# Performance work log

Measured on AMD Instinct MI355X. Metric: run time of the kernel, lower is better.

## Reference

```python
import jax, jax.numpy as jnp
import numpy as np

B, S, D, H = 4, 2048, 512, 8
DH = D // H  # 64


def setup_inputs() -> dict:
    key = jax.random.key(0)
    ks = jax.random.split(key, 7)
    scale = 1.0 / np.sqrt(D)
    return {
        "in_query": jax.random.normal(ks[0], (B, S, D), dtype=jnp.float32),
        "in_key": jax.random.normal(ks[1], (B, S, D), dtype=jnp.float32),
        "in_value": jax.random.normal(ks[2], (B, S, D), dtype=jnp.float32),
        "W_q": jax.random.normal(ks[3], (D, D), dtype=jnp.float32) * scale,
        "W_k": jax.random.normal(ks[4], (D, D), dtype=jnp.float32) * scale,
        "W_v": jax.random.normal(ks[5], (D, D), dtype=jnp.float32) * scale,
        "W_out": jax.random.normal(ks[6], (D, D), dtype=jnp.float32) * scale,
    }


def _split_heads(x):
    # [B, S, D] -> [B, H, S, DH]
    return x.reshape(B, S, H, DH).transpose(0, 2, 1, 3)


def reference(in_query, in_key, in_value, W_q, W_k, W_v, W_out):
    q = _split_heads(in_query @ W_q)   # [B,H,S,DH]
    k = _split_heads(in_key @ W_k)
    v = _split_heads(in_value @ W_v)
    scores = jnp.einsum("bhqd,bhkd->bhqk", q, k) / jnp.sqrt(jnp.float32(DH))
    attn = jax.nn.softmax(scores, axis=-1)  # dropout p=0 -> identity
    out = jnp.einsum("bhqk,bhkd->bhqd", attn, v)  # [B,H,S,DH]
    out = out.transpose(0, 2, 1, 3).reshape(B, S, D)
    return out @ W_out
```

## Files before the change

### kernel.cpp

```cpp
#include <hip/hip_runtime.h>
#include <hip/hip_bf16.h>
#include <cstdint>
#include <cstddef>


typedef __bf16 bf16;
typedef __attribute__((ext_vector_type(8))) __bf16 bf16x8;
typedef __attribute__((ext_vector_type(4))) __bf16 bf16x4;
typedef __attribute__((ext_vector_type(4))) float floatx4;

#define MFMA16(a, b, c) __builtin_amdgcn_mfma_f32_16x16x32_bf16(a, b, c, 0, 0, 0)

#define GLD16(gp, lp)                                              \
  __builtin_amdgcn_global_load_lds(                                \
      (const __attribute__((address_space(1))) unsigned int*)(gp), \
      (__attribute__((address_space(3))) unsigned int*)(lp), 16, 0, 0)

#define PIPE_TOP()                                     \
  do {                                                 \
    asm volatile("s_waitcnt vmcnt(0)" ::: "memory");   \
    __builtin_amdgcn_s_barrier();                      \
    __builtin_amdgcn_sched_barrier(0);                 \
  } while (0)

#define LGKM_BARRIER()                                 \
  do {                                                 \
    asm volatile("s_waitcnt lgkmcnt(0)" ::: "memory"); \
    __builtin_amdgcn_sched_barrier(0);                 \
    __builtin_amdgcn_s_barrier();                      \
    __builtin_amdgcn_sched_barrier(0);                 \
  } while (0)

__device__ __forceinline__ void split2(float x, bf16& hi, bf16& lo) {
  hi = (bf16)x;
  lo = (bf16)(x - (float)hi);
}

__global__ __launch_bounds__(256) void k_split_w(
    const float* __restrict__ Wq, const float* __restrict__ Wk,
    const float* __restrict__ Wv, const float* __restrict__ Wo,
    bf16* __restrict__ wt_hi, bf16* __restrict__ wt_lo) {
  __shared__ float tile[64][65];
  const int w = blockIdx.z;
  const float* W = (w == 0) ? Wq : (w == 1) ? Wk : (w == 2) ? Wv : Wo;
  const int kb = blockIdx.y * 64, nb = blockIdx.x * 64;
  const int tid = threadIdx.x;
  const int col = tid & 63, rbase = tid >> 6;
#pragma unroll
  for (int i = 0; i < 16; i++) {
    int row = rbase + i * 4;
    tile[row][col] = W[(size_t)(kb + row) * 512 + nb + col];
  }
  __syncthreads();
#pragma unroll
  for (int i = 0; i < 16; i++) {
    int nrow = rbase + i * 4;
    float v = tile[col][nrow];
    bf16 hi, lo;
    split2(v, hi, lo);
    size_t o = (size_t)w * 262144 + (size_t)(nb + nrow) * 512 + (kb + col);
    wt_hi[o] = hi;
    wt_lo[o] = lo;
  }
}

__global__ __launch_bounds__(256) void k_split_x(
    const float* __restrict__ Xq, const float* __restrict__ Xk,
    const float* __restrict__ Xv,
    bf16* __restrict__ Xh, bf16* __restrict__ Xl) {
  const int total = 3 * 1048576;
  for (int j = blockIdx.x * blockDim.x + threadIdx.x; j < total;
       j += gridDim.x * blockDim.x) {
    int w = j >> 20, off = j & 1048575;
    const float* X = (w == 0) ? Xq : (w == 1) ? Xk : Xv;
    floatx4 v = *(const floatx4*)(X + (size_t)off * 4);
    bf16x4 hv, lv;
#pragma unroll
    for (int r = 0; r < 4; r++) {
      bf16 h, l;
      split2(v[r], h, l);
      hv[r] = h; lv[r] = l;
    }
    *(bf16x4*)(Xh + (size_t)w * 4194304 + (size_t)off * 4) = hv;
    *(bf16x4*)(Xl + (size_t)w * 4194304 + (size_t)off * 4) = lv;
  }
}

__global__ __launch_bounds__(256, 3) void k_proj_qkv(
    const bf16* __restrict__ Xh, const bf16* __restrict__ Xl,
    const bf16* __restrict__ wt_hi, const bf16* __restrict__ wt_lo,
    bf16* __restrict__ Q_hi, bf16* __restrict__ Q_lo,
    bf16* __restrict__ K, bf16* __restrict__ Vt) {
  const int P = blockIdx.x;
  const int c_all = P >> 5, within = P & 31;
  const int n_idx = within >> 3, i8 = within & 7;
  const int which = c_all >> 3;
  const int g = ((c_all & 7) << 3) | i8;
  const int m0 = g * 128, n0 = n_idx * 128;

  const uint8_t* Ahb = (const uint8_t*)(Xh + (size_t)which * 4194304);
  const uint8_t* Alb = (const uint8_t*)(Xl + (size_t)which * 4194304);
  const uint8_t* Bhb = (const uint8_t*)(wt_hi + (size_t)which * 262144);
  const uint8_t* Blb = (const uint8_t*)(wt_lo + (size_t)which * 262144);
  const int tid = threadIdx.x, wave = tid >> 6, lane = tid & 63;
  const int l15 = lane & 15, l4 = lane >> 4;
  const int Am0 = (wave & 1) * 64, Bn0 = (wave >> 1) * 64;

  __shared__ bf16 sAh[128 * 32], sAl[128 * 32];
  __shared__ bf16 sBh[128 * 32], sBl[128 * 32];

  int aoff[2], boff[2], dstp[2];
#pragma unroll
  for (int p = 0; p < 2; p++) {
    int slot = p * 256 + tid;
    int row = slot >> 2, phys = slot & 3, lg = phys ^ (row & 3);
    aoff[p] = (m0 + row) * 1024 + lg * 16;
    boff[p] = (n0 + row) * 1024 + lg * 16;
    dstp[p] = slot * 16;
  }

  floatx4 acc[4][4];
#pragma unroll
  for (int i = 0; i < 4; i++)
#pragma unroll
    for (int j = 0; j < 4; j++) acc[i][j] = {0.f, 0.f, 0.f, 0.f};

#pragma unroll
  for (int p = 0; p < 2; p++) {
    GLD16(Ahb + aoff[p], (char*)sAh + dstp[p]);
    GLD16(Alb + aoff[p], (char*)sAl + dstp[p]);
    GLD16(Bhb + boff[p], (char*)sBh + dstp[p]);
    GLD16(Blb + boff[p], (char*)sBl + dstp[p]);
  }

  for (int kb = 0; kb < 512; kb += 32) {
    PIPE_TOP();

    bf16x8 ah[4], al[4], bhf[4], blf[4];
#pragma unroll
    for (int mt = 0; mt < 4; mt++) {
      int row = Am0 + mt * 16 + l15, r3 = row & 3;
      ah[mt] = *(const bf16x8*)((const char*)sAh + row * 64 + ((l4 ^ r3) * 16));
      al[mt] = *(const bf16x8*)((const char*)sAl + row * 64 + ((l4 ^ r3) * 16));
    }
#pragma unroll
    for (int nt = 0; nt < 4; nt++) {
      int row = Bn0 + nt * 16 + l15, r3 = row & 3;
      bhf[nt] = *(const bf16x8*)((const char*)sBh + row * 64 + ((l4 ^ r3) * 16));
      blf[nt] = *(const bf16x8*)((const char*)sBl + row * 64 + ((l4 ^ r3) * 16));
    }

    LGKM_BARRIER();

    if (kb + 32 < 512) {
      const int nkb = kb + 32;
#pragma unroll
      for (int p = 0; p < 2; p++) {
        GLD16(Ahb + aoff[p] + nkb * 2, (char*)sAh + dstp[p]);
        GLD16(Alb + aoff[p] + nkb * 2, (char*)sAl + dstp[p]);
        GLD16(Bhb + boff[p] + nkb * 2, (char*)sBh + dstp[p]);
        GLD16(Blb + boff[p] + nkb * 2, (char*)sBl + dstp[p]);
      }
    }

    __builtin_amdgcn_s_setprio(1);
#pragma unroll
    for (int nt = 0; nt < 4; nt++) {
#pragma unroll
      for (int mt = 0; mt < 4; mt++) {
        acc[mt][nt] = MFMA16(ah[mt], bhf[nt], acc[mt][nt]);
        acc[mt][nt] = MFMA16(ah[mt], blf[nt], acc[mt][nt]);
        acc[mt][nt] = MFMA16(al[mt], bhf[nt], acc[mt][nt]);
      }
    }
    __builtin_amdgcn_s_setprio(0);
  }

  const float scale = (which == 0) ? 0.125f : (which == 1) ? 1.44269504f : 1.0f;
#pragma unroll
  for (int mt = 0; mt < 4; mt++) {
#pragma unroll
    for (int nt = 0; nt < 4; nt++) {
      int m_base = m0 + Am0 + mt * 16 + l4 * 4;
      int n = n0 + Bn0 + nt * 16 + l15;
      int h = (n >> 6) & 7, d = n & 63;
      if (which == 2) {
        int kbase = m_base & 2047, b = m_base >> 11;
        int a32 = kbase & ~31, v = (kbase >> 2) & 7;
        int sbase = a32 + 8 * (v & 3) + 4 * (v >> 2);
        bf16x4 pv;
#pragma unroll
        for (int r = 0; r < 4; r++) pv[r] = (bf16)acc[mt][nt][r];
        *(bf16x4*)&Vt[((size_t)(b * 8 + h) * 64 + d) * 2048 + sbase] = pv;
      } else {
#pragma unroll
        for (int r = 0; r < 4; r++) {
          int m = m_base + r;
          int b = m >> 11, s = m & 2047;
          float v = acc[mt][nt][r] * scale;
          size_t o = ((size_t)(b * 8 + h) * 2048 + s) * 64 + d;
          if (which == 0) {
            bf16 hi, lo;
            split2(v, hi, lo);
            Q_hi[o] = hi; Q_lo[o] = lo;
          } else {
            K[o] = (bf16)v;
          }
        }
      }
    }
  }
}

__global__ __launch_bounds__(256, 2) void k_flash(
    const bf16* __restrict__ Q_hi, const bf16* __restrict__ Q_lo,
    const bf16* __restrict__ K, const bf16* __restrict__ Vt,
    bf16* __restrict__ O_hi, bf16* __restrict__ O_lo) {
  const int P = blockIdx.x;
  const int hi4 = P >> 8, rem = P & 255;
  const int qt = rem >> 3;
  const int bh = hi4 * 8 + (rem & 7);
  const int b = bh >> 3, h = bh & 7;
  const int tid = threadIdx.x, wave = tid >> 6, lane = tid & 63;
  const int l15 = lane & 15, l4 = lane >> 4;
  const int q0 = qt * 64;

  __shared__ char smem[2 * 32768 + 1024];
  float* lbuf = (float*)(smem + 65536);

  const uint8_t* Kb = (const uint8_t*)K + (size_t)bh * 2048 * 128;
  const uint8_t* Vb = (const uint8_t*)Vt + (size_t)bh * 64 * 4096;
  int koff[4], voff[4], dst[4];
#pragma unroll
  for (int p = 0; p < 4; p++) {
    int slot = p * 256 + tid;
    {
      int row = slot >> 3, phys = slot & 7, lg = phys ^ (row & 7);
      koff[p] = row * 128 + lg * 16;
    }
    {
      int row = slot >> 4, phys = slot & 15, lg = phys ^ (row & 15);
      voff[p] = row * 4096 + lg * 16;
    }
    dst[p] = slot * 16;
  }

#pragma unroll
  for (int p = 0; p < 4; p++) {
    GLD16(Kb + koff[p], smem + dst[p]);
    GLD16(Vb + voff[p], smem + 16384 + dst[p]);
  }

  bf16x8 qh[4][2], ql[4][2];
#pragma unroll
  for (int nt = 0; nt < 4; nt++) {
    const bf16* ph = Q_hi + ((size_t)bh * 2048 + q0 + nt * 16 + l15) * 64 + l4 * 8;
    const bf16* pl = Q_lo + ((size_t)bh * 2048 + q0 + nt * 16 + l15) * 64 + l4 * 8;
    qh[nt][0] = *(const bf16x8*)ph;
    qh[nt][1] = *(const bf16x8*)(ph + 32);
    ql[nt][0] = *(const bf16x8*)pl;
    ql[nt][1] = *(const bf16x8*)(pl + 32);
  }

  float lp[4] = {0.f, 0.f, 0.f, 0.f};
  floatx4 oacc[4][4];
#pragma unroll
  for (int i = 0; i < 4; i++)
#pragma unroll
    for (int j = 0; j < 4; j++) oacc[i][j] = {0.f, 0.f, 0.f, 0.f};

  int cur = 0;
  for (int j0 = 0; j0 < 2048; j0 += 128) {
    PIPE_TOP();

    const char* sK = smem + cur * 32768;
    const char* sV = sK + 16384;

    bf16x8 kf[2][2];
#pragma unroll
    for (int kt = 0; kt < 2; kt++) {
      int row = wave * 32 + kt * 16 + l15, r7 = row & 7;
#pragma unroll
      for (int ks = 0; ks < 2; ks++)
        kf[ks][kt] =
            *(const bf16x8*)(sK + row * 128 + (((ks * 4 + l4) ^ r7) * 16));
    }
    bf16x8 vf[4];
#pragma unroll
    for (int nt = 0; nt < 4; nt++) {
      int row = nt * 16 + l15;
      vf[nt] =
          *(const bf16x8*)(sV + row * 256 + (((wave * 4 + l4) ^ l15) * 16));
    }

    if (j0 + 128 < 2048) {
      char* nb = smem + (cur ^ 1) * 32768;
      const size_t nj = (size_t)(j0 + 128);
#pragma unroll
      for (int p = 0; p < 4; p++) {
        GLD16(Kb + nj * 128 + koff[p], nb + dst[p]);
        GLD16(Vb + nj * 2 + voff[p], nb + 16384 + dst[p]);
      }
    }

    floatx4 sc[2][4];
#pragma unroll
    for (int kt = 0; kt < 2; kt++)
#pragma unroll
      for (int nt = 0; nt < 4; nt++)
        sc[kt][nt] = {-24.f, -24.f, -24.f, -24.f};
#pragma unroll
    for (int ks = 0; ks < 2; ks++) {
#pragma unroll
      for (int nt = 0; nt < 4; nt++) {
        sc[0][nt] = MFMA16(kf[ks][0], qh[nt][ks], sc[0][nt]);
        sc[0][nt] = MFMA16(kf[ks][0], ql[nt][ks], sc[0][nt]);
        sc[1][nt] = MFMA16(kf[ks][1], qh[nt][ks], sc[1][nt]);
        sc[1][nt] = MFMA16(kf[ks][1], ql[nt][ks], sc[1][nt]);
      }
    }

    bf16x8 pf[4];
#pragma unroll
    for (int nt = 0; nt < 4; nt++) {
#pragma unroll
      for (int r = 0; r < 4; r++) {
        float p0 = __builtin_amdgcn_exp2f(sc[0][nt][r]);
        float p1 = __builtin_amdgcn_exp2f(sc[1][nt][r]);
        lp[nt] += p0 + p1;
        pf[nt][r] = (bf16)p0;
        pf[nt][4 + r] = (bf16)p1;
      }
    }

#pragma unroll
    for (int nt = 0; nt < 4; nt++) {
#pragma unroll
      for (int mq = 0; mq < 4; mq++)
        oacc[mq][nt] = MFMA16(pf[mq], vf[nt], oacc[mq][nt]);
    }
    cur ^= 1;
  }

#pragma unroll
  for (int nt = 0; nt < 4; nt++) {
    lp[nt] += __shfl_xor(lp[nt], 16, 64);
    lp[nt] += __shfl_xor(lp[nt], 32, 64);
  }
  __syncthreads();

  if (l4 == 0) {
#pragma unroll
    for (int nt = 0; nt < 4; nt++) lbuf[wave * 64 + nt * 16 + l15] = lp[nt];
  }
  floatx4* red = (floatx4*)smem;
#pragma unroll
  for (int mq = 0; mq < 4; mq++) {
    if (mq != wave) {
#pragma unroll
      for (int nt = 0; nt < 4; nt++)
        red[(wave * 16 + mq * 4 + nt) * 64 + lane] = oacc[mq][nt];
    }
  }
  __syncthreads();

  {
    const int mq = wave;
    floatx4 fin[4];
#pragma unroll
    for (int nt = 0; nt < 4; nt++) {
      floatx4 s0 = (wave == 0) ? oacc[mq][nt]
                               : red[(0 * 16 + mq * 4 + nt) * 64 + lane];
      floatx4 s1 = (wave == 1) ? oacc[mq][nt]
                               : red[(1 * 16 + mq * 4 + nt) * 64 + lane];
      floatx4 s2 = (wave == 2) ? oacc[mq][nt]
                               : red[(2 * 16 + mq * 4 + nt) * 64 + lane];
      floatx4 s3 = (wave == 3) ? oacc[mq][nt]
                               : red[(3 * 16 + mq * 4 + nt) * 64 + lane];
      fin[nt] = s0 + ((s1 + s2) + s3);
    }
    float ltw = lbuf[mq * 16 + l15] + lbuf[64 + mq * 16 + l15] +
                lbuf[128 + mq * 16 + l15] + lbuf[192 + mq * 16 + l15];
    float rlw[4];
#pragma unroll
    for (int r = 0; r < 4; r++)
      rlw[r] = 1.0f / __shfl(ltw, (lane & 48) | (l4 * 4 + r), 64);
#pragma unroll
    for (int nt = 0; nt < 4; nt++) {
#pragma unroll
      for (int r = 0; r < 4; r++) {
        float v = fin[nt][r] * rlw[r];
        int gs = q0 + mq * 16 + l4 * 4 + r;
        int gd = h * 64 + nt * 16 + l15;
        size_t o = ((size_t)b * 2048 + gs) * 512 + gd;
        bf16 hi, lo;
        split2(v, hi, lo);
        O_hi[o] = hi;
        O_lo[o] = lo;
      }
    }
  }
}

__global__ __launch_bounds__(256, 2) void k_proj_out(
    const bf16* __restrict__ O_hi, const bf16* __restrict__ O_lo,
    const bf16* __restrict__ wt_hi, const bf16* __restrict__ wt_lo,
    float* __restrict__ out) {
  const int P = blockIdx.x;
  const int g = P & 127, n_idx = P >> 7;
  const int m0 = g * 64, n0 = n_idx * 128;

  const uint8_t* Ahb = (const uint8_t*)O_hi;
  const uint8_t* Alb = (const uint8_t*)O_lo;
  const uint8_t* Bhb = (const uint8_t*)(wt_hi + (size_t)3 * 262144);
  const uint8_t* Blb = (const uint8_t*)(wt_lo + (size_t)3 * 262144);
  const int tid = threadIdx.x, wave = tid >> 6, lane = tid & 63;
  const int l15 = lane & 15, l4 = lane >> 4;
  const int Am0 = (wave & 1) * 32, Bn0 = (wave >> 1) * 64;

  __shared__ bf16 sAh[64 * 32], sAl[64 * 32];
  __shared__ bf16 sBh[128 * 32], sBl[128 * 32];

  int aoff, adst;
  {
    int slot = tid;
    int row = slot >> 2, phys = slot & 3, lg = phys ^ (row & 3);
    aoff = (m0 + row) * 1024 + lg * 16;
    adst = slot * 16;
  }
  int boff[2], bdst[2];
#pragma unroll
  for (int p = 0; p < 2; p++) {
    int slot = p * 256 + tid;
    int row = slot >> 2, phys = slot & 3, lg = phys ^ (row & 3);
    boff[p] = (n0 + row) * 1024 + lg * 16;
    bdst[p] = slot * 16;
  }

  floatx4 acc[2][4];
#pragma unroll
  for (int i = 0; i < 2; i++)
#pragma unroll
    for (int j = 0; j < 4; j++) acc[i][j] = {0.f, 0.f, 0.f, 0.f};

  GLD16(Ahb + aoff, (char*)sAh + adst);
  GLD16(Alb + aoff, (char*)sAl + adst);
#pragma unroll
  for (int p = 0; p < 2; p++) {
    GLD16(Bhb + boff[p], (char*)sBh + bdst[p]);
    GLD16(Blb + boff[p], (char*)sBl + bdst[p]);
  }

  for (int kb = 0; kb < 512; kb += 32) {
    PIPE_TOP();

    bf16x8 ah[2], al[2], bhf[4], blf[4];
#pragma unroll
    for (int mt = 0; mt < 2; mt++) {
      int row = Am0 + mt * 16 + l15, r3 = row & 3;
      ah[mt] = *(const bf16x8*)((const char*)sAh + row * 64 + ((l4 ^ r3) * 16));
      al[mt] = *(const bf16x8*)((const char*)sAl + row * 64 + ((l4 ^ r3) * 16));
    }
#pragma unroll
    for (int nt = 0; nt < 4; nt++) {
      int row = Bn0 + nt * 16 + l15, r3 = row & 3;
      bhf[nt] = *(const bf16x8*)((const char*)sBh + row * 64 + ((l4 ^ r3) * 16));
      blf[nt] = *(const bf16x8*)((const char*)sBl + row * 64 + ((l4 ^ r3) * 16));
    }

    LGKM_BARRIER();

    if (kb + 32 < 512) {
      const int nkb = kb + 32;
      GLD16(Ahb + aoff + nkb * 2, (char*)sAh + adst);
      GLD16(Alb + aoff + nkb * 2, (char*)sAl + adst);
#pragma unroll
      for (int p = 0; p < 2; p++) {
        GLD16(Bhb + boff[p] + nkb * 2, (char*)sBh + bdst[p]);
        GLD16(Blb + boff[p] + nkb * 2, (char*)sBl + bdst[p]);
      }
    }

    __builtin_amdgcn_s_setprio(1);
#pragma unroll
    for (int nt = 0; nt < 4; nt++) {
#pragma unroll
      for (int mt = 0; mt < 2; mt++) {
        acc[mt][nt] = MFMA16(ah[mt], bhf[nt], acc[mt][nt]);
        acc[mt][nt] = MFMA16(ah[mt], blf[nt], acc[mt][nt]);
        acc[mt][nt] = MFMA16(al[mt], bhf[nt], acc[mt][nt]);
      }
    }
    __builtin_amdgcn_s_setprio(0);
  }
#pragma unroll
  for (int mt = 0; mt < 2; mt++) {
#pragma unroll
    for (int nt = 0; nt < 4; nt++) {
#pragma unroll
      for (int r = 0; r < 4; r++) {
        int m = m0 + Am0 + mt * 16 + l4 * 4 + r;
        int n = n0 + Bn0 + nt * 16 + l15;
        out[(size_t)m * 512 + n] = acc[mt][nt][r];
      }
    }
  }
}

extern "C" void kernel_launch(void* const* d_in, const int* in_sizes, int n_in,
                              void* d_out, int out_size, void* d_ws, size_t ws_size,
                              hipStream_t stream) {
  (void)in_sizes; (void)n_in; (void)out_size; (void)ws_size;
  const float* Xq = (const float*)d_in[0];
  const float* Xk = (const float*)d_in[1];
  const float* Xv = (const float*)d_in[2];
  const float* Wq = (const float*)d_in[3];
  const float* Wk = (const float*)d_in[4];
  const float* Wv = (const float*)d_in[5];
  const float* Wo = (const float*)d_in[6];
  float* out = (float*)d_out;

  char* ws = (char*)d_ws;
  size_t off = 0;
  auto alloc = [&](size_t n) {
    void* p = ws + off;
    off += (n + 255) & ~(size_t)255;
    return p;
  };
  const size_t NW = 4 * 262144;
  const size_t NE = 4194304;
  const size_t NX = 3 * 4194304;
  bf16* wt_hi = (bf16*)alloc(NW * 2);
  bf16* wt_lo = (bf16*)alloc(NW * 2);
  bf16* Qh = (bf16*)alloc(NE * 2);
  bf16* Ql = (bf16*)alloc(NE * 2);
  bf16* Kk = (bf16*)alloc(NE * 2);
  bf16* Vt = (bf16*)alloc(NE * 2);
  char* shared_region = (char*)alloc(2 * NX * 2);
  bf16* Xh = (bf16*)shared_region;
  bf16* Xl = Xh + NX;
  bf16* Oh = (bf16*)shared_region;
  bf16* Ol = Oh + NE;

  k_split_w<<<dim3(8, 8, 4), dim3(256), 0, stream>>>(Wq, Wk, Wv, Wo, wt_hi, wt_lo);
  k_split_x<<<dim3(2048), dim3(256), 0, stream>>>(Xq, Xk, Xv, Xh, Xl);
  k_proj_qkv<<<dim3(768), dim3(256), 0, stream>>>(Xh, Xl, wt_hi, wt_lo,
                                                  Qh, Ql, Kk, Vt);
  k_flash<<<dim3(1024), dim3(256), 0, stream>>>(Qh, Ql, Kk, Vt, Oh, Ol);
  k_proj_out<<<dim3(512), dim3(256), 0, stream>>>(Oh, Ol, wt_hi, wt_lo, out);
}
```

Baseline: 220.6 us.

## Split flash waves into 2x2 query/key halves with smaller KV tiles

Reorganizes the flash-attention block so its four waves form a 2x2 grid over query halves and key halves, replacing the layout where every wave covered all 64 queries. The KV tile per iteration drops from 128 to 64 keys, which halves LDS use and shrinks the cross-wave reduction to a pairwise sum. Occupancy is raised to three blocks per CU. The trade-off is twice as many loop iterations and barriers, and each K fragment is now reused across fewer query tiles.

```diff
diff --git a/kernel.cpp b/kernel.cpp
--- a/kernel.cpp
+++ b/kernel.cpp
@@ -212,7 +212,7 @@
   }
 }
 
-__global__ __launch_bounds__(256, 2) void k_flash(
+__global__ __launch_bounds__(256, 3) void k_flash(
     const bf16* __restrict__ Q_hi, const bf16* __restrict__ Q_lo,
     const bf16* __restrict__ K, const bf16* __restrict__ Vt,
     bf16* __restrict__ O_hi, bf16* __restrict__ O_lo) {
@@ -224,62 +224,60 @@
   const int tid = threadIdx.x, wave = tid >> 6, lane = tid & 63;
   const int l15 = lane & 15, l4 = lane >> 4;
   const int q0 = qt * 64;
-
-  __shared__ char smem[2 * 32768 + 1024];
-  float* lbuf = (float*)(smem + 65536);
+  const int qh = wave >> 1, kh = wave & 1;
+
+  __shared__ char smem[2 * 16384 + 512];
+  float* lbuf = (float*)(smem + 32768);
 
   const uint8_t* Kb = (const uint8_t*)K + (size_t)bh * 2048 * 128;
   const uint8_t* Vb = (const uint8_t*)Vt + (size_t)bh * 64 * 4096;
-  int koff[4], voff[4], dst[4];
-#pragma unroll
-  for (int p = 0; p < 4; p++) {
+  int koff[2], voff[2], dst2[2];
+#pragma unroll
+  for (int p = 0; p < 2; p++) {
     int slot = p * 256 + tid;
-    {
-      int row = slot >> 3, phys = slot & 7, lg = phys ^ (row & 7);
-      koff[p] = row * 128 + lg * 16;
-    }
-    {
-      int row = slot >> 4, phys = slot & 15, lg = phys ^ (row & 15);
-      voff[p] = row * 4096 + lg * 16;
-    }
-    dst[p] = slot * 16;
-  }
-
-#pragma unroll
-  for (int p = 0; p < 4; p++) {
-    GLD16(Kb + koff[p], smem + dst[p]);
-    GLD16(Vb + voff[p], smem + 16384 + dst[p]);
-  }
-
-  bf16x8 qh[4][2], ql[4][2];
-#pragma unroll
-  for (int nt = 0; nt < 4; nt++) {
-    const bf16* ph = Q_hi + ((size_t)bh * 2048 + q0 + nt * 16 + l15) * 64 + l4 * 8;
-    const bf16* pl = Q_lo + ((size_t)bh * 2048 + q0 + nt * 16 + l15) * 64 + l4 * 8;
-    qh[nt][0] = *(const bf16x8*)ph;
-    qh[nt][1] = *(const bf16x8*)(ph + 32);
-    ql[nt][0] = *(const bf16x8*)pl;
-    ql[nt][1] = *(const bf16x8*)(pl + 32);
-  }
-
-  float lp[4] = {0.f, 0.f, 0.f, 0.f};
-  floatx4 oacc[4][4];
-#pragma unroll
-  for (int i = 0; i < 4; i++)
+    int row = slot >> 3, phys = slot & 7, lg = phys ^ (row & 7);
+    koff[p] = row * 128 + lg * 16;
+    voff[p] = row * 4096 + lg * 16;
+    dst2[p] = slot * 16;
+  }
+
+#pragma unroll
+  for (int p = 0; p < 2; p++) {
+    GLD16(Kb + koff[p], smem + dst2[p]);
+    GLD16(Vb + voff[p], smem + 8192 + dst2[p]);
+  }
+
+  bf16x8 qhf[2][2], qlf[2][2];
+#pragma unroll
+  for (int nt = 0; nt < 2; nt++) {
+    const bf16* ph =
+        Q_hi + ((size_t)bh * 2048 + q0 + qh * 32 + nt * 16 + l15) * 64 + l4 * 8;
+    const bf16* pl =
+        Q_lo + ((size_t)bh * 2048 + q0 + qh * 32 + nt * 16 + l15) * 64 + l4 * 8;
+    qhf[nt][0] = *(const bf16x8*)ph;
+    qhf[nt][1] = *(const bf16x8*)(ph + 32);
+    qlf[nt][0] = *(const bf16x8*)pl;
+    qlf[nt][1] = *(const bf16x8*)(pl + 32);
+  }
+
+  float lp[2] = {0.f, 0.f};
+  floatx4 oacc[2][4];
+#pragma unroll
+  for (int i = 0; i < 2; i++)
 #pragma unroll
     for (int j = 0; j < 4; j++) oacc[i][j] = {0.f, 0.f, 0.f, 0.f};
 
   int cur = 0;
-  for (int j0 = 0; j0 < 2048; j0 += 128) {
+  for (int j0 = 0; j0 < 2048; j0 += 64) {
     PIPE_TOP();
 
-    const char* sK = smem + cur * 32768;
-    const char* sV = sK + 16384;
+    const char* sK = smem + cur * 16384;
+    const char* sV = sK + 8192;
 
     bf16x8 kf[2][2];
 #pragma unroll
     for (int kt = 0; kt < 2; kt++) {
-      int row = wave * 32 + kt * 16 + l15, r7 = row & 7;
+      int row = kh * 32 + kt * 16 + l15, r7 = row & 7;
 #pragma unroll
       for (int ks = 0; ks < 2; ks++)
         kf[ks][kt] =
@@ -289,40 +287,40 @@
 #pragma unroll
     for (int nt = 0; nt < 4; nt++) {
       int row = nt * 16 + l15;
-      vf[nt] =
-          *(const bf16x8*)(sV + row * 256 + (((wave * 4 + l4) ^ l15) * 16));
-    }
-
-    if (j0 + 128 < 2048) {
-      char* nb = smem + (cur ^ 1) * 32768;
-      const size_t nj = (size_t)(j0 + 128);
-#pragma unroll
-      for (int p = 0; p < 4; p++) {
-        GLD16(Kb + nj * 128 + koff[p], nb + dst[p]);
-        GLD16(Vb + nj * 2 + voff[p], nb + 16384 + dst[p]);
-      }
-    }
-
-    floatx4 sc[2][4];
+      vf[nt] = *(const bf16x8*)(sV + row * 128 +
+                                (((kh * 4 + l4) ^ (row & 7)) * 16));
+    }
+
+    if (j0 + 64 < 2048) {
+      char* nb = smem + (cur ^ 1) * 16384;
+      const size_t nj = (size_t)(j0 + 64);
+#pragma unroll
+      for (int p = 0; p < 2; p++) {
+        GLD16(Kb + nj * 128 + koff[p], nb + dst2[p]);
+        GLD16(Vb + nj * 2 + voff[p], nb + 8192 + dst2[p]);
+      }
+    }
+
+    floatx4 sc[2][2];
 #pragma unroll
     for (int kt = 0; kt < 2; kt++)
 #pragma unroll
-      for (int nt = 0; nt < 4; nt++)
+      for (int nt = 0; nt < 2; nt++)
         sc[kt][nt] = {-24.f, -24.f, -24.f, -24.f};
 #pragma unroll
     for (int ks = 0; ks < 2; ks++) {
 #pragma unroll
-      for (int nt = 0; nt < 4; nt++) {
-        sc[0][nt] = MFMA16(kf[ks][0], qh[nt][ks], sc[0][nt]);
-        sc[0][nt] = MFMA16(kf[ks][0], ql[nt][ks], sc[0][nt]);
-        sc[1][nt] = MFMA16(kf[ks][1], qh[nt][ks], sc[1][nt]);
-        sc[1][nt] = MFMA16(kf[ks][1], ql[nt][ks], sc[1][nt]);
-      }
-    }
-
-    bf16x8 pf[4];
-#pragma unroll
-    for (int nt = 0; nt < 4; nt++) {
+      for (int nt = 0; nt < 2; nt++) {
+        sc[0][nt] = MFMA16(kf[ks][0], qhf[nt][ks], sc[0][nt]);
+        sc[0][nt] = MFMA16(kf[ks][0], qlf[nt][ks], sc[0][nt]);
+        sc[1][nt] = MFMA16(kf[ks][1], qhf[nt][ks], sc[1][nt]);
+        sc[1][nt] = MFMA16(kf[ks][1], qlf[nt][ks], sc[1][nt]);
+      }
+    }
+
+    bf16x8 pf[2];
+#pragma unroll
+    for (int nt = 0; nt < 2; nt++) {
 #pragma unroll
       for (int r = 0; r < 4; r++) {
         float p0 = __builtin_amdgcn_exp2f(sc[0][nt][r]);
@@ -336,14 +334,14 @@
 #pragma unroll
     for (int nt = 0; nt < 4; nt++) {
 #pragma unroll
-      for (int mq = 0; mq < 4; mq++)
+      for (int mq = 0; mq < 2; mq++)
         oacc[mq][nt] = MFMA16(pf[mq], vf[nt], oacc[mq][nt]);
     }
     cur ^= 1;
   }
 
 #pragma unroll
-  for (int nt = 0; nt < 4; nt++) {
+  for (int nt = 0; nt < 2; nt++) {
     lp[nt] += __shfl_xor(lp[nt], 16, 64);
     lp[nt] += __shfl_xor(lp[nt], 32, 64);
   }
@@ -351,52 +349,41 @@
 
   if (l4 == 0) {
 #pragma unroll
-    for (int nt = 0; nt < 4; nt++) lbuf[wave * 64 + nt * 16 + l15] = lp[nt];
+    for (int nt = 0; nt < 2; nt++) lbuf[wave * 32 + nt * 16 + l15] = lp[nt];
   }
   floatx4* red = (floatx4*)smem;
-#pragma unroll
-  for (int mq = 0; mq < 4; mq++) {
-    if (mq != wave) {
+  if (kh == 1) {
+#pragma unroll
+    for (int mq = 0; mq < 2; mq++)
 #pragma unroll
       for (int nt = 0; nt < 4; nt++)
-        red[(wave * 16 + mq * 4 + nt) * 64 + lane] = oacc[mq][nt];
-    }
+        red[((qh * 2 + mq) * 4 + nt) * 64 + lane] = oacc[mq][nt];
   }
   __syncthreads();
 
-  {
-    const int mq = wave;
-    floatx4 fin[4];
-#pragma unroll
-    for (int nt = 0; nt < 4; nt++) {
-      floatx4 s0 = (wave == 0) ? oacc[mq][nt]
-                               : red[(0 * 16 + mq * 4 + nt) * 64 + lane];
-      floatx4 s1 = (wave == 1) ? oacc[mq][nt]
-                               : red[(1 * 16 + mq * 4 + nt) * 64 + lane];
-      floatx4 s2 = (wave == 2) ? oacc[mq][nt]
-                               : red[(2 * 16 + mq * 4 + nt) * 64 + lane];
-      floatx4 s3 = (wave == 3) ? oacc[mq][nt]
-                               : red[(3 * 16 + mq * 4 + nt) * 64 + lane];
-      fin[nt] = s0 + ((s1 + s2) + s3);
-    }
-    float ltw = lbuf[mq * 16 + l15] + lbuf[64 + mq * 16 + l15] +
-                lbuf[128 + mq * 16 + l15] + lbuf[192 + mq * 16 + l15];
-    float rlw[4];
-#pragma unroll
-    for (int r = 0; r < 4; r++)
-      rlw[r] = 1.0f / __shfl(ltw, (lane & 48) | (l4 * 4 + r), 64);
-#pragma unroll
-    for (int nt = 0; nt < 4; nt++) {
-#pragma unroll
-      for (int r = 0; r < 4; r++) {
-        float v = fin[nt][r] * rlw[r];
-        int gs = q0 + mq * 16 + l4 * 4 + r;
-        int gd = h * 64 + nt * 16 + l15;
-        size_t o = ((size_t)b * 2048 + gs) * 512 + gd;
-        bf16 hi, lo;
-        split2(v, hi, lo);
-        O_hi[o] = hi;
-        O_lo[o] = lo;
+  if (kh == 0) {
+#pragma unroll
+    for (int mq = 0; mq < 2; mq++) {
+      float ltw = lbuf[(qh * 2 + 0) * 32 + mq * 16 + l15] +
+                  lbuf[(qh * 2 + 1) * 32 + mq * 16 + l15];
+      float rlw[4];
+#pragma unroll
+      for (int r = 0; r < 4; r++)
+        rlw[r] = 1.0f / __shfl(ltw, (lane & 48) | (l4 * 4 + r), 64);
+#pragma unroll
+      for (int nt = 0; nt < 4; nt++) {
+        floatx4 fin = oacc[mq][nt] + red[((qh * 2 + mq) * 4 + nt) * 64 + lane];
+#pragma unroll
+        for (int r = 0; r < 4; r++) {
+          float v = fin[r] * rlw[r];
+          int gs = q0 + qh * 32 + mq * 16 + l4 * 4 + r;
+          int gd = h * 64 + nt * 16 + l15;
+          size_t o = ((size_t)b * 2048 + gs) * 512 + gd;
+          bf16 hi, lo;
+          split2(v, hi, lo);
+          O_hi[o] = hi;
+          O_lo[o] = lo;
+        }
       }
     }
   }
```

Result: no change. 222.0 us (+0.6%).

## Give each wave private K/V LDS buffers to drop block-wide barriers

Applied to the files above, without the earlier changes.

Each wave now loads only the 32-key slice of K and V it consumes into its own double-buffered LDS region, with a matching per-wave swizzle. The per-iteration block barrier is replaced by a wave-local vmcnt wait. This removes cross-wave synchronisation stalls in the flash loop. In exchange each wave issues its own smaller loads, and the V layout and swizzle change, which risks more bank conflicts or less coalesced global reads.

```diff
diff --git a/kernel.cpp b/kernel.cpp
--- a/kernel.cpp
+++ b/kernel.cpp
@@ -20,6 +20,12 @@
   do {                                                 \
     asm volatile("s_waitcnt vmcnt(0)" ::: "memory");   \
     __builtin_amdgcn_s_barrier();                      \
+    __builtin_amdgcn_sched_barrier(0);                 \
+  } while (0)
+
+#define WAVE_VM_WAIT()                                 \
+  do {                                                 \
+    asm volatile("s_waitcnt vmcnt(0)" ::: "memory");   \
     __builtin_amdgcn_sched_barrier(0);                 \
   } while (0)
 
@@ -225,30 +231,31 @@
   const int l15 = lane & 15, l4 = lane >> 4;
   const int q0 = qt * 64;
 
-  __shared__ char smem[2 * 32768 + 1024];
+  __shared__ char smem[65536 + 1024];
   float* lbuf = (float*)(smem + 65536);
+  char* wbase = smem + wave * 16384;
 
   const uint8_t* Kb = (const uint8_t*)K + (size_t)bh * 2048 * 128;
   const uint8_t* Vb = (const uint8_t*)Vt + (size_t)bh * 64 * 4096;
-  int koff[4], voff[4], dst[4];
+
+  int koff[4], voff[4], dstk[4];
 #pragma unroll
   for (int p = 0; p < 4; p++) {
-    int slot = p * 256 + tid;
-    {
-      int row = slot >> 3, phys = slot & 7, lg = phys ^ (row & 7);
-      koff[p] = row * 128 + lg * 16;
-    }
-    {
-      int row = slot >> 4, phys = slot & 15, lg = phys ^ (row & 15);
-      voff[p] = row * 4096 + lg * 16;
-    }
-    dst[p] = slot * 16;
-  }
-
-#pragma unroll
-  for (int p = 0; p < 4; p++) {
-    GLD16(Kb + koff[p], smem + dst[p]);
-    GLD16(Vb + voff[p], smem + 16384 + dst[p]);
+    int slot = p * 64 + lane;
+    int krow = slot >> 3, kphys = slot & 7, klg = kphys ^ (krow & 7);
+    koff[p] = krow * 128 + klg * 16;
+    int vrow = slot >> 2, vphys = slot & 3, vlg = vphys ^ (vrow & 3);
+    voff[p] = vrow * 4096 + vlg * 16;
+    dstk[p] = slot * 16;
+  }
+
+  {
+    const size_t j0 = (size_t)wave * 32;
+#pragma unroll
+    for (int p = 0; p < 4; p++) {
+      GLD16(Kb + j0 * 128 + koff[p], wbase + dstk[p]);
+      GLD16(Vb + j0 * 2 + voff[p], wbase + 4096 + dstk[p]);
+    }
   }
 
   bf16x8 qh[4][2], ql[4][2];
@@ -270,36 +277,35 @@
     for (int j = 0; j < 4; j++) oacc[i][j] = {0.f, 0.f, 0.f, 0.f};
 
   int cur = 0;
-  for (int j0 = 0; j0 < 2048; j0 += 128) {
-    PIPE_TOP();
-
-    const char* sK = smem + cur * 32768;
-    const char* sV = sK + 16384;
+  for (int t = 0; t < 16; t++) {
+    WAVE_VM_WAIT();
+
+    const char* kbuf = wbase + cur * 8192;
+    const char* vbuf = kbuf + 4096;
 
     bf16x8 kf[2][2];
 #pragma unroll
     for (int kt = 0; kt < 2; kt++) {
-      int row = wave * 32 + kt * 16 + l15, r7 = row & 7;
+      int row = kt * 16 + l15, r7 = row & 7;
 #pragma unroll
       for (int ks = 0; ks < 2; ks++)
         kf[ks][kt] =
-            *(const bf16x8*)(sK + row * 128 + (((ks * 4 + l4) ^ r7) * 16));
+            *(const bf16x8*)(kbuf + row * 128 + (((ks * 4 + l4) ^ r7) * 16));
     }
     bf16x8 vf[4];
 #pragma unroll
     for (int nt = 0; nt < 4; nt++) {
       int row = nt * 16 + l15;
-      vf[nt] =
-          *(const bf16x8*)(sV + row * 256 + (((wave * 4 + l4) ^ l15) * 16));
-    }
-
-    if (j0 + 128 < 2048) {
-      char* nb = smem + (cur ^ 1) * 32768;
-      const size_t nj = (size_t)(j0 + 128);
+      vf[nt] = *(const bf16x8*)(vbuf + row * 64 + ((l4 ^ (row & 3)) * 16));
+    }
+
+    if (t + 1 < 16) {
+      char* nb = wbase + (cur ^ 1) * 8192;
+      const size_t nj = (size_t)(t + 1) * 128 + (size_t)wave * 32;
 #pragma unroll
       for (int p = 0; p < 4; p++) {
-        GLD16(Kb + nj * 128 + koff[p], nb + dst[p]);
-        GLD16(Vb + nj * 2 + voff[p], nb + 16384 + dst[p]);
+        GLD16(Kb + nj * 128 + koff[p], nb + dstk[p]);
+        GLD16(Vb + nj * 2 + voff[p], nb + 4096 + dstk[p]);
       }
     }
 
```

After: 250.9 us. 1.14x slower.
